# Kernel optimization log

Measured on AMD Instinct MI355X. Metric: run time of the kernel, lower is better.

The kernel has to match this reference:

```python
import math
import jax, jax.numpy as jnp
import numpy as np

D_MODEL = 512
N_STATE = 64
L_SEQ = 2048


def setup_inputs() -> dict:
    key = jax.random.key(0)
    k1, k2, k3, k4, k5 = jax.random.split(key, 5)
    log_A_real = jnp.log(0.5 * jnp.ones((D_MODEL, N_STATE), dtype=jnp.float32))
    A_imag = jnp.pi * jnp.arange(N_STATE, dtype=jnp.float32) / N_STATE
    B_re = jax.random.normal(k1, (D_MODEL, N_STATE), dtype=jnp.float32)
    B_im = jax.random.normal(k2, (D_MODEL, N_STATE), dtype=jnp.float32)
    C_re = jax.random.normal(k3, (D_MODEL, N_STATE), dtype=jnp.float32)
    C_im = jax.random.normal(k4, (D_MODEL, N_STATE), dtype=jnp.float32)
    lo, hi = math.log(0.001), math.log(0.1)
    log_dt = jax.random.uniform(k5, (D_MODEL,), dtype=jnp.float32) * (hi - lo) + lo
    return {
        "length": L_SEQ,
        "log_A_real": log_A_real,
        "A_imag": A_imag,
        "B_re": B_re,
        "B_im": B_im,
        "C_re": C_re,
        "C_im": C_im,
        "log_dt": log_dt,
    }


def reference(length, log_A_real, A_imag, B_re, B_im, C_re, C_im, log_dt):
    # dt: (d_model, 1)
    dt = jnp.exp(log_dt)[:, None]
    # A: (d_model, N) complex64
    A = -jnp.exp(log_A_real) + 1j * A_imag
    # discretized pole: A_bar = exp(A * dt), (d_model, N)
    A_bar = jnp.exp(A * dt)
    B = B_re + 1j * B_im  # (d_model, N)
    C = C_re + 1j * C_im  # (d_model, N)
    # NOTE: original code computes B_bar = B*dt but never uses it; kernel uses B.
    t = jnp.arange(length, dtype=jnp.float32)  # (L,)
    # Vandermonde powers: (d_model, L, N) complex — the large intermediate
    A_powers = A_bar[:, None, :] ** t[None, :, None]
    # K[d, l] = sum_n C[d,n] * B[d,n] * A_bar[d,n]^l  -> (d_model, L)
    K = jnp.sum(C[:, None, :] * B[:, None, :] * A_powers, axis=-1)
    return K
```

## Files before the change

kernel.cpp:

```cpp
#include <hip/hip_runtime.h>
#include <math.h>

#define D_MODEL 512
#define N_STATE 64
#define L_SEQ   2048
#define BLOCK   256
#define CHUNK   (L_SEQ / BLOCK)

template <bool COMPLEX_OUT>
__global__ __launch_bounds__(BLOCK) void ssm_vandermonde_kernel(
    const float* __restrict__ log_A_real,
    const float* __restrict__ A_imag,
    const float* __restrict__ B_re,
    const float* __restrict__ B_im,
    const float* __restrict__ C_re,
    const float* __restrict__ C_im,
    const float* __restrict__ log_dt,
    float* __restrict__ out)
{
    __shared__ float sh_a [N_STATE];
    __shared__ float sh_th[N_STATE];
    __shared__ float sh_sr[N_STATE];
    __shared__ float sh_si[N_STATE];
    __shared__ float sh_wr[N_STATE];
    __shared__ float sh_wi[N_STATE];

    const int d = blockIdx.x;
    const int t = threadIdx.x;

    if (t < N_STATE) {
        const int n   = t;
        const int idx = d * N_STATE + n;
        const float dt = expf(log_dt[d]);
        const float a  = expf(log_A_real[idx]) * dt;
        const float th = A_imag[n] * dt;
        const float r  = expf(-a);
        float s, c;
        sincosf(th, &s, &c);
        sh_a [n] = a;
        sh_th[n] = th;
        sh_sr[n] = r * c;
        sh_si[n] = r * s;
        const float br = B_re[idx], bi = B_im[idx];
        const float cr = C_re[idx], ci = C_im[idx];
        sh_wr[n] = cr * br - ci * bi;
        sh_wi[n] = cr * bi + ci * br;
    }
    __syncthreads();

    float accr[CHUNK], acci[CHUNK];
#pragma unroll
    for (int j = 0; j < CHUNK; ++j) { accr[j] = 0.0f; acci[j] = 0.0f; }

    const int   l0  = t * CHUNK;
    const float fl0 = (float)l0;

    for (int n = 0; n < N_STATE; ++n) {
        const float mag = expf(-sh_a[n] * fl0);
        const float ang = sh_th[n] * fl0;
        float s, c;
        sincosf(ang, &s, &c);
        float pr = mag * c;
        float pi = mag * s;
        const float sr = sh_sr[n], si = sh_si[n];
        const float wr = sh_wr[n], wi = sh_wi[n];
#pragma unroll
        for (int j = 0; j < CHUNK; ++j) {
            accr[j] = fmaf(wr, pr, fmaf(-wi, pi, accr[j]));
            acci[j] = fmaf(wr, pi, fmaf( wi, pr, acci[j]));
            const float npr = fmaf(pr, sr, -(pi * si));
            const float npi = fmaf(pr, si,   pi * sr);
            pr = npr;
            pi = npi;
        }
    }

    if (COMPLEX_OUT) {
        float4* o = (float4*)(out + 2u * ((size_t)d * L_SEQ + l0));
#pragma unroll
        for (int j = 0; j < CHUNK; j += 2) {
            o[j / 2] = make_float4(accr[j], acci[j], accr[j + 1], acci[j + 1]);
        }
    } else {
        float4* o = (float4*)(out + (size_t)d * L_SEQ + l0);
#pragma unroll
        for (int j = 0; j < CHUNK; j += 4) {
            o[j / 4] = make_float4(accr[j], accr[j + 1], accr[j + 2], accr[j + 3]);
        }
    }
}

extern "C" void kernel_launch(void* const* d_in, const int* in_sizes, int n_in,
                              void* d_out, int out_size, void* d_ws, size_t ws_size,
                              hipStream_t stream) {
    const float* log_A_real = (const float*)d_in[1];
    const float* A_imag     = (const float*)d_in[2];
    const float* B_re       = (const float*)d_in[3];
    const float* B_im       = (const float*)d_in[4];
    const float* C_re       = (const float*)d_in[5];
    const float* C_im       = (const float*)d_in[6];
    const float* log_dt     = (const float*)d_in[7];
    float* out = (float*)d_out;

    dim3 grid(D_MODEL), block(BLOCK);
    if (out_size >= 2 * D_MODEL * L_SEQ) {
        ssm_vandermonde_kernel<true><<<grid, block, 0, stream>>>(
            log_A_real, A_imag, B_re, B_im, C_re, C_im, log_dt, out);
    } else {
        ssm_vandermonde_kernel<false><<<grid, block, 0, stream>>>(
            log_A_real, A_imag, B_re, B_im, C_re, C_im, log_dt, out);
    }
}
```

Before: 90.35 us.

## Split power recurrence into two stride-two chains and process two states per iteration

Each state's power sequence is now advanced with the squared pole, so even and odd positions form two independent recurrence chains. This shortens the serial dependency chain inside the chunk loop. Two states are handled per outer iteration to expose more instruction-level parallelism. The precise expf/sincosf in the per-thread start powers are replaced with the fast __expf/__sincosf intrinsics, which lowers transcendental cost but may reduce accuracy at large arguments.

```diff
diff --git a/kernel.cpp b/kernel.cpp
--- a/kernel.cpp
+++ b/kernel.cpp
@@ -18,12 +18,14 @@
     const float* __restrict__ log_dt,
     float* __restrict__ out)
 {
-    __shared__ float sh_a [N_STATE];
-    __shared__ float sh_th[N_STATE];
-    __shared__ float sh_sr[N_STATE];
-    __shared__ float sh_si[N_STATE];
-    __shared__ float sh_wr[N_STATE];
-    __shared__ float sh_wi[N_STATE];
+    __shared__ float sh_a  [N_STATE];
+    __shared__ float sh_th [N_STATE];
+    __shared__ float sh_sr [N_STATE];
+    __shared__ float sh_si [N_STATE];
+    __shared__ float sh_s2r[N_STATE];
+    __shared__ float sh_s2i[N_STATE];
+    __shared__ float sh_wr [N_STATE];
+    __shared__ float sh_wi [N_STATE];
 
     const int d = blockIdx.x;
     const int t = threadIdx.x;
@@ -34,13 +36,18 @@
         const float dt = expf(log_dt[d]);
         const float a  = expf(log_A_real[idx]) * dt;
         const float th = A_imag[n] * dt;
-        const float r  = expf(-a);
         float s, c;
         sincosf(th, &s, &c);
+        const float r = expf(-a);
         sh_a [n] = a;
         sh_th[n] = th;
         sh_sr[n] = r * c;
         sh_si[n] = r * s;
+        float s2, c2;
+        sincosf(2.0f * th, &s2, &c2);
+        const float r2 = expf(-2.0f * a);
+        sh_s2r[n] = r2 * c2;
+        sh_s2i[n] = r2 * s2;
         const float br = B_re[idx], bi = B_im[idx];
         const float cr = C_re[idx], ci = C_im[idx];
         sh_wr[n] = cr * br - ci * bi;
@@ -55,23 +62,45 @@
     const int   l0  = t * CHUNK;
     const float fl0 = (float)l0;
 
-    for (int n = 0; n < N_STATE; ++n) {
-        const float mag = expf(-sh_a[n] * fl0);
-        const float ang = sh_th[n] * fl0;
-        float s, c;
-        sincosf(ang, &s, &c);
-        float pr = mag * c;
-        float pi = mag * s;
-        const float sr = sh_sr[n], si = sh_si[n];
-        const float wr = sh_wr[n], wi = sh_wi[n];
+    for (int n = 0; n < N_STATE; n += 2) {
+        float s0, c0, s1, c1;
+        const float mag0 = __expf(-sh_a[n]     * fl0);
+        const float mag1 = __expf(-sh_a[n + 1] * fl0);
+        __sincosf(sh_th[n]     * fl0, &s0, &c0);
+        __sincosf(sh_th[n + 1] * fl0, &s1, &c1);
+        float p0r = mag0 * c0, p0i = mag0 * s0;
+        float p1r = mag1 * c1, p1i = mag1 * s1;
+        const float sr0 = sh_sr[n],     si0 = sh_si[n];
+        const float sr1 = sh_sr[n + 1], si1 = sh_si[n + 1];
+        float q0r = fmaf(p0r, sr0, -(p0i * si0));
+        float q0i = fmaf(p0r, si0,   p0i * sr0);
+        float q1r = fmaf(p1r, sr1, -(p1i * si1));
+        float q1i = fmaf(p1r, si1,   p1i * sr1);
+        const float e0r = sh_s2r[n],     e0i = sh_s2i[n];
+        const float e1r = sh_s2r[n + 1], e1i = sh_s2i[n + 1];
+        const float w0r = sh_wr[n],      w0i = sh_wi[n];
+        const float w1r = sh_wr[n + 1],  w1i = sh_wi[n + 1];
+
 #pragma unroll
-        for (int j = 0; j < CHUNK; ++j) {
-            accr[j] = fmaf(wr, pr, fmaf(-wi, pi, accr[j]));
-            acci[j] = fmaf(wr, pi, fmaf( wi, pr, acci[j]));
-            const float npr = fmaf(pr, sr, -(pi * si));
-            const float npi = fmaf(pr, si,   pi * sr);
-            pr = npr;
-            pi = npi;
+        for (int j = 0; j < CHUNK; j += 2) {
+            accr[j]     = fmaf(w0r, p0r, fmaf(-w0i, p0i, accr[j]));
+            acci[j]     = fmaf(w0r, p0i, fmaf( w0i, p0r, acci[j]));
+            accr[j]     = fmaf(w1r, p1r, fmaf(-w1i, p1i, accr[j]));
+            acci[j]     = fmaf(w1r, p1i, fmaf( w1i, p1r, acci[j]));
+            accr[j + 1] = fmaf(w0r, q0r, fmaf(-w0i, q0i, accr[j + 1]));
+            acci[j + 1] = fmaf(w0r, q0i, fmaf( w0i, q0r, acci[j + 1]));
+            accr[j + 1] = fmaf(w1r, q1r, fmaf(-w1i, q1i, accr[j + 1]));
+            acci[j + 1] = fmaf(w1r, q1i, fmaf( w1i, q1r, acci[j + 1]));
+            const float np0r = fmaf(p0r, e0r, -(p0i * e0i));
+            const float np0i = fmaf(p0r, e0i,   p0i * e0r);
+            const float nq0r = fmaf(q0r, e0r, -(q0i * e0i));
+            const float nq0i = fmaf(q0r, e0i,   q0i * e0r);
+            const float np1r = fmaf(p1r, e1r, -(p1i * e1i));
+            const float np1i = fmaf(p1r, e1i,   p1i * e1r);
+            const float nq1r = fmaf(q1r, e1r, -(q1i * e1i));
+            const float nq1i = fmaf(q1r, e1i,   q1i * e1r);
+            p0r = np0r; p0i = np0i; q0r = nq0r; q0i = nq0i;
+            p1r = np1r; p1i = np1i; q1r = nq1r; q1i = nq1i;
         }
     }
 
```

After: 78.62 us. 13.0% less time.

## Pack state pairs into float2 vectors and fold weights into the power recurrence

Applied to the files above, without the earlier changes.

Processes two state indices at once using 2-wide float vectors, so the compiler can emit packed FP32 math. The C*B weight is premultiplied into the running power, which turns the per-step accumulation into plain adds. Even and odd positions advance as two independent chains with a squared step, which shortens the dependency chain. Per-thread setup switches to fast __expf/__sincosf intrinsics, which may lose some accuracy over the long recurrence.

```diff
diff --git a/kernel.cpp b/kernel.cpp
--- a/kernel.cpp
+++ b/kernel.cpp
@@ -6,6 +6,12 @@
 #define L_SEQ   2048
 #define BLOCK   256
 #define CHUNK   (L_SEQ / BLOCK)
+
+typedef float v2f __attribute__((ext_vector_type(2)));
+
+static __device__ __forceinline__ v2f mk2(float a, float b) {
+    v2f r; r.x = a; r.y = b; return r;
+}
 
 template <bool COMPLEX_OUT>
 __global__ __launch_bounds__(BLOCK) void ssm_vandermonde_kernel(
@@ -18,12 +24,14 @@
     const float* __restrict__ log_dt,
     float* __restrict__ out)
 {
-    __shared__ float sh_a [N_STATE];
-    __shared__ float sh_th[N_STATE];
-    __shared__ float sh_sr[N_STATE];
-    __shared__ float sh_si[N_STATE];
-    __shared__ float sh_wr[N_STATE];
-    __shared__ float sh_wi[N_STATE];
+    __shared__ v2f sh_a  [N_STATE / 2];
+    __shared__ v2f sh_th [N_STATE / 2];
+    __shared__ v2f sh_s1r[N_STATE / 2];
+    __shared__ v2f sh_s1i[N_STATE / 2];
+    __shared__ v2f sh_e2r[N_STATE / 2];
+    __shared__ v2f sh_e2i[N_STATE / 2];
+    __shared__ v2f sh_wr [N_STATE / 2];
+    __shared__ v2f sh_wi [N_STATE / 2];
 
     const int d = blockIdx.x;
     const int t = threadIdx.x;
@@ -34,45 +42,69 @@
         const float dt = expf(log_dt[d]);
         const float a  = expf(log_A_real[idx]) * dt;
         const float th = A_imag[n] * dt;
-        const float r  = expf(-a);
         float s, c;
         sincosf(th, &s, &c);
-        sh_a [n] = a;
-        sh_th[n] = th;
-        sh_sr[n] = r * c;
-        sh_si[n] = r * s;
+        const float r = expf(-a);
+        float s2, c2;
+        sincosf(2.0f * th, &s2, &c2);
+        const float r2 = expf(-2.0f * a);
         const float br = B_re[idx], bi = B_im[idx];
         const float cr = C_re[idx], ci = C_im[idx];
-        sh_wr[n] = cr * br - ci * bi;
-        sh_wi[n] = cr * bi + ci * br;
+        ((float*)sh_a  )[n] = a;
+        ((float*)sh_th )[n] = th;
+        ((float*)sh_s1r)[n] = r * c;
+        ((float*)sh_s1i)[n] = r * s;
+        ((float*)sh_e2r)[n] = r2 * c2;
+        ((float*)sh_e2i)[n] = r2 * s2;
+        ((float*)sh_wr )[n] = cr * br - ci * bi;
+        ((float*)sh_wi )[n] = cr * bi + ci * br;
     }
     __syncthreads();
 
-    float accr[CHUNK], acci[CHUNK];
+    v2f avr[CHUNK], avi[CHUNK];
 #pragma unroll
-    for (int j = 0; j < CHUNK; ++j) { accr[j] = 0.0f; acci[j] = 0.0f; }
+    for (int j = 0; j < CHUNK; ++j) { avr[j] = mk2(0.f, 0.f); avi[j] = mk2(0.f, 0.f); }
 
     const int   l0  = t * CHUNK;
     const float fl0 = (float)l0;
 
-    for (int n = 0; n < N_STATE; ++n) {
-        const float mag = expf(-sh_a[n] * fl0);
-        const float ang = sh_th[n] * fl0;
-        float s, c;
-        sincosf(ang, &s, &c);
-        float pr = mag * c;
-        float pi = mag * s;
-        const float sr = sh_sr[n], si = sh_si[n];
-        const float wr = sh_wr[n], wi = sh_wi[n];
+    for (int np = 0; np < N_STATE / 2; ++np) {
+        const v2f a2  = sh_a [np];
+        const v2f th2 = sh_th[np];
+        float s0, c0, s1, c1;
+        const float mag0 = __expf(-a2.x * fl0);
+        const float mag1 = __expf(-a2.y * fl0);
+        __sincosf(th2.x * fl0, &s0, &c0);
+        __sincosf(th2.y * fl0, &s1, &c1);
+        const v2f pr = mk2(mag0 * c0, mag1 * c1);
+        const v2f pi = mk2(mag0 * s0, mag1 * s1);
+        const v2f wr = sh_wr[np], wi = sh_wi[np];
+        v2f uer = wr * pr - wi * pi;
+        v2f uei = wr * pi + wi * pr;
+        const v2f s1r = sh_s1r[np], s1i = sh_s1i[np];
+        v2f uor = uer * s1r - uei * s1i;
+        v2f uoi = uer * s1i + uei * s1r;
+        const v2f er = sh_e2r[np], ei = sh_e2i[np];
+
 #pragma unroll
-        for (int j = 0; j < CHUNK; ++j) {
-            accr[j] = fmaf(wr, pr, fmaf(-wi, pi, accr[j]));
-            acci[j] = fmaf(wr, pi, fmaf( wi, pr, acci[j]));
-            const float npr = fmaf(pr, sr, -(pi * si));
-            const float npi = fmaf(pr, si,   pi * sr);
-            pr = npr;
-            pi = npi;
+        for (int j = 0; j < CHUNK; j += 2) {
+            avr[j]     += uer;
+            avi[j]     += uei;
+            avr[j + 1] += uor;
+            avi[j + 1] += uoi;
+            const v2f ner = uer * er - uei * ei;
+            const v2f nei = uer * ei + uei * er;
+            const v2f nor_ = uor * er - uoi * ei;
+            const v2f noi  = uor * ei + uoi * er;
+            uer = ner; uei = nei; uor = nor_; uoi = noi;
         }
+    }
+
+    float accr[CHUNK], acci[CHUNK];
+#pragma unroll
+    for (int j = 0; j < CHUNK; ++j) {
+        accr[j] = avr[j].x + avr[j].y;
+        acci[j] = avi[j].x + avi[j].y;
     }
 
     if (COMPLEX_OUT) {
```

After: 76.40 us. -15.4%, faster.
